# Optimization experiments

Hardware: AMD Instinct MI355X
Metric: run time of the kernel (lower is better)

The kernel has to match this reference:

```python
import jax, jax.numpy as jnp
import numpy as np

K, N, M = 65536, 4096, 64  # observations, basis centers, features


def setup_inputs() -> dict:
    key = jax.random.key(0)
    k1, k2, k3, k4 = jax.random.split(key, 4)
    x = jax.random.normal(k1, (K, M), dtype=jnp.float32)
    x_basis = jax.random.normal(k2, (N, M), dtype=jnp.float32)
    w = jax.random.normal(k3, (1, N), dtype=jnp.float32) / np.sqrt(N)
    b = jax.random.normal(k4, (1,), dtype=jnp.float32)
    return {"x": x, "x_basis": x_basis, "w": w, "b": b}


def reference(x, x_basis, w, b):
    # pairwise squared distances ||x_i - c_j||^2, [K, N]
    x2 = jnp.sum(x * x, axis=1, keepdims=True)          # [K, 1]
    c2 = jnp.sum(x_basis * x_basis, axis=1)             # [N]
    sq = x2 + c2[None, :] - 2.0 * (x @ x_basis.T)       # [K, N]
    phi = jnp.exp(-sq)                                  # gaussian RBF
    return jax.nn.sigmoid(phi @ w.T + b)                # [K, 1]
```

## Files before the change

kernel.cpp:

```cpp
#include <hip/hip_runtime.h>


#define KOBS 65536
#define NCENT 4096
#define MFEAT 64
#define NCHUNK 32

#define SCALE_A 2.8853900817779268f
#define QS      1.4426950408889634f
#define TSKIP   -60.0f

typedef __attribute__((ext_vector_type(4)))  float float4v;
typedef __attribute__((ext_vector_type(16))) float float16v;
typedef __attribute__((ext_vector_type(8)))  int   int8v;

#if __has_builtin(__builtin_amdgcn_exp2f)
#define EXP2F(x) __builtin_amdgcn_exp2f(x)
#else
#define EXP2F(x) exp2f(x)
#endif

static __device__ inline unsigned f2bfu(float f) {
    unsigned u = __float_as_uint(f);
    return (u + 0x7fffu + ((u >> 16) & 1u)) >> 16;
}

#define MFMA(A, B, C) __builtin_amdgcn_mfma_scale_f32_32x32x64_f8f6f4( \
    (A), (B), (C), 0, 0, 0, 0x7f7f7f7f, 0, 0x7f7f7f7f)

#define MAX16(DST, AV) do {                                        \
    float t0_ = fmaxf(fmaxf((AV)[0],  (AV)[1]),  (AV)[2]);         \
    float t1_ = fmaxf(fmaxf((AV)[3],  (AV)[4]),  (AV)[5]);         \
    float t2_ = fmaxf(fmaxf((AV)[6],  (AV)[7]),  (AV)[8]);         \
    float t3_ = fmaxf(fmaxf((AV)[9],  (AV)[10]), (AV)[11]);        \
    float t4_ = fmaxf(fmaxf((AV)[12], (AV)[13]), (AV)[14]);        \
    DST = fmaxf(fmaxf(fmaxf(t0_, t1_), t2_),                       \
                fmaxf(fmaxf(t3_, t4_), (AV)[15]));                 \
} while (0)

__global__ __launch_bounds__(256) void rbf_prep(
    const float* __restrict__ xb, const float* __restrict__ w,
    char* __restrict__ cb, unsigned* __restrict__ hcw) {
    const int bid = blockIdx.x;
    const int tid = threadIdx.x;
    if (bid < 128) {
        const int o      = bid * 256 + tid;
        const int col    = o >> 3;
        const int joct   = o & 7;
        const int c      = col >> 7;
        const int w4     = (col >> 5) & 3;
        const int lanelo = col & 31;
        const int l      = lanelo + (joct >> 2) * 32;
        const int j0     = (joct & 3) * 8;
        const float* src = xb + col * MFEAT + joct * 8;
        float4v v0 = *(const float4v*)(src);
        float4v v1 = *(const float4v*)(src + 4);
        int lo = __builtin_amdgcn_cvt_pk_fp8_f32(v0[0], v0[1], 0, false);
        lo     = __builtin_amdgcn_cvt_pk_fp8_f32(v0[2], v0[3], lo, true);
        int hi = __builtin_amdgcn_cvt_pk_fp8_f32(v1[0], v1[1], 0, false);
        hi     = __builtin_amdgcn_cvt_pk_fp8_f32(v1[2], v1[3], hi, true);
        unsigned long long pk = (unsigned long long)(unsigned)lo |
                                ((unsigned long long)(unsigned)hi << 32);
        *(unsigned long long*)(cb + (size_t)((c * 4 + w4) * 64 + l) * 32 + j0) = pk;
    } else {
        const int row  = (bid - 128) * 4 + (tid >> 6);
        const int lane = tid & 63;
        float v = xb[row * MFEAT + lane];
        float s = v * v;
        #pragma unroll
        for (int off = 32; off > 0; off >>= 1) s += __shfl_xor(s, off, 64);
        if (lane == 0)
            hcw[row] = (f2bfu(TSKIP + QS * s) << 16) | f2bfu(w[row]);
    }
}

__global__ __launch_bounds__(256, 6) void rbf_main(
    const float* __restrict__ x, const char* __restrict__ cb,
    const unsigned* __restrict__ hcw, const float* __restrict__ bptr,
    float* __restrict__ out) {
    __shared__ float x2s[32];
    __shared__ float zl[32];

    const int tid  = threadIdx.x;
    const int wq   = tid >> 6;
    const int lane = tid & 63;
    const int ll   = lane & 31;
    const int lh   = lane >> 5;
    const int bid  = (int)blockIdx.x;
    const int rb   = 4 * lh;

    if (tid < 32) zl[tid] = 0.0f;

    int8v af;
    {
        const float* xr = x + (size_t)(bid * 32 + ll) * MFEAT + lh * 32;
        float ss = 0.0f;
        #pragma unroll
        for (int rg = 0; rg < 8; ++rg) {
            float4v v = *(const float4v*)(xr + rg * 4);
            ss = fmaf(v[0], v[0], ss); ss = fmaf(v[1], v[1], ss);
            ss = fmaf(v[2], v[2], ss); ss = fmaf(v[3], v[3], ss);
            int pk = __builtin_amdgcn_cvt_pk_fp8_f32(
                SCALE_A * v[0], SCALE_A * v[1], 0, false);
            pk = __builtin_amdgcn_cvt_pk_fp8_f32(
                SCALE_A * v[2], SCALE_A * v[3], pk, true);
            af[rg] = pk;
        }
        ss += __shfl_xor(ss, 32, 64);
        if (wq == 0 && lh == 0) x2s[ll] = ss;
    }
    __syncthreads();

    float16v p;
    #pragma unroll
    for (int i = 0; i < 16; ++i)
        p[i] = -QS * x2s[rb + (i & 3) + 8 * (i >> 2)];

    const unsigned cboff = (unsigned)(wq * 64 + lane) * 32u;
    const unsigned moff  = (unsigned)(wq * 32 + ll);

    int8v    pb0, pb1;
    unsigned mw0, mw1;

    pb0 = *(const int8v*)(cb + cboff);
    mw0 = hcw[moff];
    pb1 = *(const int8v*)(cb + cboff + 8192u);
    mw1 = hcw[moff + 128u];

    #define STEP(C, PB, MW) do {                                           \
        const float tq  = __uint_as_float(MW & 0xffff0000u);               \
        const float wv_ = __uint_as_float(MW << 16);                       \
        float16v d = MFMA(af, PB, p);                                      \
        if ((C) + 2 < NCHUNK) {                                            \
            PB = *(const int8v*)(cb + cboff + (unsigned)((C) + 2) * 8192u);\
            MW = hcw[moff + (unsigned)((C) + 2) * 128u];                   \
        }                                                                  \
        float mx;                                                          \
        MAX16(mx, d);                                                      \
        if (__any(mx > tq)) {                    \
            if (mx > tq) {                                                 \
                const float q = TSKIP - tq;          \
                _Pragma("unroll")                                          \
                for (int i_ = 0; i_ < 16; ++i_)                            \
                    atomicAdd(&zl[rb + (i_ & 3) + 8 * (i_ >> 2)],          \
                              wv_ * EXP2F(d[i_] + q));                     \
            }                                                              \
        }                                                                  \
    } while (0)

    #pragma unroll 1
    for (int c = 0; c < NCHUNK; c += 2) {
        STEP(c,     pb0, mw0);
        STEP(c + 1, pb1, mw1);
    }

    #undef STEP

    __syncthreads();
    if (tid < 32) {
        const float z = zl[tid] + bptr[0];
        out[bid * 32 + tid] = 1.0f / (1.0f + EXP2F(-QS * z));
    }
}

extern "C" void kernel_launch(void* const* d_in, const int* in_sizes, int n_in,
                              void* d_out, int out_size, void* d_ws, size_t ws_size,
                              hipStream_t stream) {
    const float* x  = (const float*)d_in[0];
    const float* xb = (const float*)d_in[1];
    const float* w  = (const float*)d_in[2];
    const float* b  = (const float*)d_in[3];
    float* out = (float*)d_out;

    char*     cb  = (char*)d_ws;
    unsigned* hcw = (unsigned*)((char*)d_ws + NCENT * MFEAT);

    rbf_prep<<<128 + NCENT / 4, 256, 0, stream>>>(xb, w, cb, hcw);
    rbf_main<<<KOBS / 32, 256, 0, stream>>>(x, cb, hcw, b, out);
}
```

Baseline: 96.44 us.

## Split centers across blocks, stage center tiles in LDS, accumulate globally

Centers are split into 8 slices of 512. Each 512-thread block covers 256 observation rows and stages its slice of fp8 centers and packed threshold/weight metadata in shared memory once, instead of every wave streaming centers from global memory. Partial RBF sums now go to a zero-initialised global buffer through global atomics, and a new epilogue kernel applies the bias and sigmoid. This trades repeated global center reads for LDS reuse, at the cost of global atomic traffic, 32 KB of LDS per block, and one extra kernel launch.

Result: no change. 95.74 us (-0.7%).

```diff
diff --git a/kernel.cpp b/kernel.cpp
--- a/kernel.cpp
+++ b/kernel.cpp
@@ -4,15 +4,18 @@
 #define KOBS 65536
 #define NCENT 4096
 #define MFEAT 64
-#define NCHUNK 32
+#define NSPLIT 8
+#define SPLITC 512
+#define NT 16
 
 #define SCALE_A 2.8853900817779268f
 #define QS      1.4426950408889634f
 #define TSKIP   -60.0f
 
-typedef __attribute__((ext_vector_type(4)))  float float4v;
-typedef __attribute__((ext_vector_type(16))) float float16v;
-typedef __attribute__((ext_vector_type(8)))  int   int8v;
+typedef __attribute__((ext_vector_type(4)))  float    float4v;
+typedef __attribute__((ext_vector_type(16))) float    float16v;
+typedef __attribute__((ext_vector_type(8)))  int      int8v;
+typedef __attribute__((ext_vector_type(4)))  unsigned uint4v;
 
 #if __has_builtin(__builtin_amdgcn_exp2f)
 #define EXP2F(x) __builtin_amdgcn_exp2f(x)
@@ -40,18 +43,13 @@
 
 __global__ __launch_bounds__(256) void rbf_prep(
     const float* __restrict__ xb, const float* __restrict__ w,
-    char* __restrict__ cb, unsigned* __restrict__ hcw) {
+    char* __restrict__ cb, unsigned* __restrict__ hcw, float* __restrict__ z) {
     const int bid = blockIdx.x;
     const int tid = threadIdx.x;
     if (bid < 128) {
-        const int o      = bid * 256 + tid;
-        const int col    = o >> 3;
-        const int joct   = o & 7;
-        const int c      = col >> 7;
-        const int w4     = (col >> 5) & 3;
-        const int lanelo = col & 31;
-        const int l      = lanelo + (joct >> 2) * 32;
-        const int j0     = (joct & 3) * 8;
+        const int o    = bid * 256 + tid;
+        const int col  = o >> 3;
+        const int joct = o & 7;
         const float* src = xb + col * MFEAT + joct * 8;
         float4v v0 = *(const float4v*)(src);
         float4v v1 = *(const float4v*)(src + 4);
@@ -61,8 +59,8 @@
         hi     = __builtin_amdgcn_cvt_pk_fp8_f32(v1[2], v1[3], hi, true);
         unsigned long long pk = (unsigned long long)(unsigned)lo |
                                 ((unsigned long long)(unsigned)hi << 32);
-        *(unsigned long long*)(cb + (size_t)((c * 4 + w4) * 64 + l) * 32 + j0) = pk;
-    } else {
+        *(unsigned long long*)(cb + (size_t)col * 64 + joct * 8) = pk;
+    } else if (bid < 128 + 1024) {
         const int row  = (bid - 128) * 4 + (tid >> 6);
         const int lane = tid & 63;
         float v = xb[row * MFEAT + lane];
@@ -71,29 +69,39 @@
         for (int off = 32; off > 0; off >>= 1) s += __shfl_xor(s, off, 64);
         if (lane == 0)
             hcw[row] = (f2bfu(TSKIP + QS * s) << 16) | f2bfu(w[row]);
+    } else {
+        float4v zero = {0.0f, 0.0f, 0.0f, 0.0f};
+        ((float4v*)z)[(bid - 1152) * 256 + tid] = zero;
     }
 }
 
-__global__ __launch_bounds__(256, 6) void rbf_main(
+__global__ __launch_bounds__(512, 6) void rbf_main(
     const float* __restrict__ x, const char* __restrict__ cb,
-    const unsigned* __restrict__ hcw, const float* __restrict__ bptr,
-    float* __restrict__ out) {
-    __shared__ float x2s[32];
-    __shared__ float zl[32];
+    const unsigned* __restrict__ hcw, float* __restrict__ z) {
+    __shared__ char     cbs[SPLITC * 64];
+    __shared__ unsigned meta_s[SPLITC];
+    __shared__ float    x2s[256];
 
     const int tid  = threadIdx.x;
-    const int wq   = tid >> 6;
+    const int wv   = tid >> 6;
     const int lane = tid & 63;
     const int ll   = lane & 31;
     const int lh   = lane >> 5;
     const int bid  = (int)blockIdx.x;
+    const int s    = bid & 7;
+    const int rowbase = (bid >> 3) * 256;
     const int rb   = 4 * lh;
 
-    if (tid < 32) zl[tid] = 0.0f;
+    const char* gsrc = cb + (size_t)s * (SPLITC * 64) + (size_t)tid * 64;
+    uint4v g0 = ((const uint4v*)gsrc)[0];
+    uint4v g1 = ((const uint4v*)gsrc)[1];
+    uint4v g2 = ((const uint4v*)gsrc)[2];
+    uint4v g3 = ((const uint4v*)gsrc)[3];
+    unsigned mstg = (tid < SPLITC) ? hcw[s * SPLITC + tid] : 0u;
 
     int8v af;
     {
-        const float* xr = x + (size_t)(bid * 32 + ll) * MFEAT + lh * 32;
+        const float* xr = x + (size_t)(rowbase + wv * 32 + ll) * MFEAT + lh * 32;
         float ss = 0.0f;
         #pragma unroll
         for (int rg = 0; rg < 8; ++rg) {
@@ -107,60 +115,63 @@
             af[rg] = pk;
         }
         ss += __shfl_xor(ss, 32, 64);
-        if (wq == 0 && lh == 0) x2s[ll] = ss;
+        if (lh == 0) x2s[wv * 32 + ll] = ss;
+    }
+
+    {
+        uint4v* ldst = (uint4v*)(cbs + tid * 64);
+        ldst[0] = g0; ldst[1] = g1; ldst[2] = g2; ldst[3] = g3;
+        if (tid < SPLITC) meta_s[tid] = mstg;
     }
     __syncthreads();
 
     float16v p;
     #pragma unroll
     for (int i = 0; i < 16; ++i)
-        p[i] = -QS * x2s[rb + (i & 3) + 8 * (i >> 2)];
+        p[i] = -QS * x2s[wv * 32 + rb + (i & 3) + 8 * (i >> 2)];
 
-    const unsigned cboff = (unsigned)(wq * 64 + lane) * 32u;
-    const unsigned moff  = (unsigned)(wq * 32 + ll);
+    const int   zrow = rowbase + wv * 32 + rb;
+    const char* cbl  = cbs + (unsigned)ll * 64 + (unsigned)lh * 32;
 
-    int8v    pb0, pb1;
-    unsigned mw0, mw1;
+    #pragma unroll 2
+    for (int t = 0; t < NT; ++t) {
+        const char* bp = cbl + t * 2048;
+        uint4v blo = *(const uint4v*)(bp);
+        uint4v bhi = *(const uint4v*)(bp + 16);
+        int8v b;
+        b[0] = (int)blo[0]; b[1] = (int)blo[1]; b[2] = (int)blo[2]; b[3] = (int)blo[3];
+        b[4] = (int)bhi[0]; b[5] = (int)bhi[1]; b[6] = (int)bhi[2]; b[7] = (int)bhi[3];
+        const unsigned mu = meta_s[t * 32 + ll];
+        const float tq  = __uint_as_float(mu & 0xffff0000u);
+        const float wv_ = __uint_as_float(mu << 16);
 
-    pb0 = *(const int8v*)(cb + cboff);
-    mw0 = hcw[moff];
-    pb1 = *(const int8v*)(cb + cboff + 8192u);
-    mw1 = hcw[moff + 128u];
+        float16v d = MFMA(af, b, p);
 
-    #define STEP(C, PB, MW) do {                                           \
-        const float tq  = __uint_as_float(MW & 0xffff0000u);               \
-        const float wv_ = __uint_as_float(MW << 16);                       \
-        float16v d = MFMA(af, PB, p);                                      \
-        if ((C) + 2 < NCHUNK) {                                            \
-            PB = *(const int8v*)(cb + cboff + (unsigned)((C) + 2) * 8192u);\
-            MW = hcw[moff + (unsigned)((C) + 2) * 128u];                   \
-        }                                                                  \
-        float mx;                                                          \
-        MAX16(mx, d);                                                      \
-        if (__any(mx > tq)) {                    \
-            if (mx > tq) {                                                 \
-                const float q = TSKIP - tq;          \
-                _Pragma("unroll")                                          \
-                for (int i_ = 0; i_ < 16; ++i_)                            \
-                    atomicAdd(&zl[rb + (i_ & 3) + 8 * (i_ >> 2)],          \
-                              wv_ * EXP2F(d[i_] + q));                     \
-            }                                                              \
-        }                                                                  \
-    } while (0)
+        float mx;
+        MAX16(mx, d);
+        if (__any(mx > tq)) {
+            if (mx > tq) {
+                const float q = TSKIP - tq;
+                #pragma unroll
+                for (int i_ = 0; i_ < 16; ++i_)
+                    atomicAdd(&z[zrow + (i_ & 3) + 8 * (i_ >> 2)],
+                              wv_ * EXP2F(d[i_] + q));
+            }
+        }
+    }
+}
 
-    #pragma unroll 1
-    for (int c = 0; c < NCHUNK; c += 2) {
-        STEP(c,     pb0, mw0);
-        STEP(c + 1, pb1, mw1);
-    }
-
-    #undef STEP
-
-    __syncthreads();
-    if (tid < 32) {
-        const float z = zl[tid] + bptr[0];
-        out[bid * 32 + tid] = 1.0f / (1.0f + EXP2F(-QS * z));
-    }
+__global__ __launch_bounds__(256) void rbf_epi(
+    const float* __restrict__ z, const float* __restrict__ bptr,
+    float* __restrict__ out) {
+    const int i = blockIdx.x * 256 + threadIdx.x;
+    const float bb = bptr[0];
+    float4v zz = ((const float4v*)z)[i];
+    float4v o;
+    #pragma unroll
+    for (int j = 0; j < 4; ++j)
+        o[j] = 1.0f / (1.0f + EXP2F(-QS * (zz[j] + bb)));
+    ((float4v*)out)[i] = o;
 }
 
 extern "C" void kernel_launch(void* const* d_in, const int* in_sizes, int n_in,
@@ -174,7 +185,9 @@
 
     char*     cb  = (char*)d_ws;
     unsigned* hcw = (unsigned*)((char*)d_ws + NCENT * MFEAT);
+    float*    z   = (float*)((char*)d_ws + NCENT * MFEAT + NCENT * 4);
 
-    rbf_prep<<<128 + NCENT / 4, 256, 0, stream>>>(xb, w, cb, hcw);
-    rbf_main<<<KOBS / 32, 256, 0, stream>>>(x, cb, hcw, b, out);
+    rbf_prep<<<128 + 1024 + 64, 256, 0, stream>>>(xb, w, cb, hcw, z);
+    rbf_main<<<(KOBS / 256) * NSPLIT, 512, 0, stream>>>(x, cb, hcw, z);
+    rbf_epi<<<KOBS / 1024, 256, 0, stream>>>(z, b, out);
 }
```
